# Kernel tuning notes

Hardware: AMD Instinct MI355X
Metric: run time of the kernel (lower is better)

Reference implementation:

```python
import jax, jax.numpy as jnp
import numpy as np

E = 768      # embedding_dim
H = 16       # max_heads
HD = E // H  # head_dim = 48


def setup_inputs() -> dict:
    key0 = jax.random.key(0)
    ks = jax.random.split(key0, 16)
    B, Lq, Lk = 4, 1024, 2048
    s = 0.02
    return {
        "query": jax.random.normal(ks[0], (B, Lq, E), jnp.float32),
        "key": jax.random.normal(ks[1], (B, Lk, E), jnp.float32),
        "value": jax.random.normal(ks[2], (B, Lk, E), jnp.float32),
        "key_padding_mask": jnp.zeros((B, Lk), jnp.bool_),
        # param_predictor: Linear(2E->E), Linear(E->E//2), Linear(E//2->3)
        "Wp1": jax.random.normal(ks[3], (E, 2 * E), jnp.float32) * s,
        "bp1": jnp.zeros((E,), jnp.float32),
        "Wp2": jax.random.normal(ks[4], (E // 2, E), jnp.float32) * s,
        "bp2": jnp.zeros((E // 2,), jnp.float32),
        "Wp3": jax.random.normal(ks[5], (3, E // 2), jnp.float32) * s,
        "bp3": jnp.zeros((3,), jnp.float32),
        # MultiheadAttention packed in-projection + out-projection
        "in_proj_w": jax.random.normal(ks[6], (3 * E, E), jnp.float32) * s,
        "in_proj_b": jnp.zeros((3 * E,), jnp.float32),
        "out_w": jax.random.normal(ks[7], (E, E), jnp.float32) * s,
        "out_b": jnp.zeros((E,), jnp.float32),
        # LayerNorm
        "ln_g": jnp.ones((E,), jnp.float32),
        "ln_b": jnp.zeros((E,), jnp.float32),
    }


def _layer_norm(x, g, b, eps=1e-5):
    mu = x.mean(-1, keepdims=True)
    var = ((x - mu) ** 2).mean(-1, keepdims=True)
    return (x - mu) * jax.lax.rsqrt(var + eps) * g + b


def reference(query, key, value, key_padding_mask,
              Wp1, bp1, Wp2, bp2, Wp3, bp3,
              in_proj_w, in_proj_b, out_w, out_b, ln_g, ln_b):
    B, Lq, _ = query.shape
    Lk = key.shape[1]

    # ---- dynamic parameter prediction MLP ----
    pin = jnp.concatenate([query.mean(1), key.mean(1)], axis=-1)  # [B, 2E]
    h = jax.nn.relu(pin @ Wp1.T + bp1)
    h = jax.nn.relu(h @ Wp2.T + bp2)
    pred = h @ Wp3.T + bp3                                        # [B, 3]
    num_heads = jnp.round(jax.nn.sigmoid(pred[:, 0]) * (H - 1) + 1).astype(jnp.int32)
    scale_factor = jax.nn.sigmoid(pred[:, 1]) * 0.5 + 0.5         # [B]
    gate_value = jax.nn.sigmoid(pred[:, 2])                       # [B]

    # ---- multihead cross-attention (non-flash: weights are materialized) ----
    q = query @ in_proj_w[:E].T + in_proj_b[:E]
    k = key @ in_proj_w[E:2 * E].T + in_proj_b[E:2 * E]
    v = value @ in_proj_w[2 * E:].T + in_proj_b[2 * E:]
    q = q.reshape(B, Lq, H, HD)
    k = k.reshape(B, Lk, H, HD)
    v = v.reshape(B, Lk, H, HD)
    scores = jnp.einsum('bqhd,bkhd->bhqk', q, k) / np.sqrt(HD)    # [B,H,Lq,Lk]
    scores = jnp.where(key_padding_mask[:, None, None, :], -1e30, scores)
    attn = jax.nn.softmax(scores, axis=-1)
    ctx = jnp.einsum('bhqk,bkhd->bqhd', attn, v).reshape(B, Lq, E)
    attn_output = ctx @ out_w.T + out_b
    attn_weights = attn.mean(1)                                   # avg over heads, [B,Lq,Lk]

    # ---- gated scale + residual + LayerNorm epilogue (dropout = eval/identity) ----
    sf = scale_factor[:, None, None]
    gv = gate_value[:, None, None]
    gated = query * (1.0 - gv) + (attn_output * sf) * gv
    output = _layer_norm(query + gated, ln_g, ln_b)
    return output, attn_weights, (num_heads, scale_factor, gate_value)
```

## Files before the change

kernel.cpp:

```cpp
#include <hip/hip_runtime.h>

#define B_ 4
#define LQ 1024
#define LK 2048
#define E_ 768
#define H_ 16
#define HD_ 48
#define HDP 64

#define OUT0_SIZE (B_*LQ*E_)
#define AW_OFF    (OUT0_SIZE)
#define AW_SIZE   (B_*LQ*LK)
#define NH_OFF    (AW_OFF + AW_SIZE)
#define SF_OFF    (NH_OFF + 4)
#define GV_OFF    (NH_OFF + 8)

#define WOFF_PIN    0
#define WOFF_QFRAG  49152
#define WOFF_KFRAG  (WOFF_QFRAG + (size_t)B_*H_*LQ*HDP*2)
#define WOFF_VFRAG  (WOFF_KFRAG + (size_t)B_*H_*LK*HDP*2)
#define WOFF_CTX    (WOFF_VFRAG + (size_t)B_*H_*HD_*LK*2)
#define WOFF_DINV   (WOFF_CTX + (size_t)B_*LQ*E_*2)
#define WOFF_H1     (WOFF_DINV + (size_t)B_*H_*LQ*4)
#define WOFF_H2     (WOFF_H1 + B_*E_*4)
#define WOFF_WBF    (WOFF_H2 + B_*(E_/2)*4)
#define WOFF_OWBF   (WOFF_WBF + (size_t)2304*768*2)
#define WOFF_AO     (WOFF_OWBF + (size_t)768*768*2)
#define WOFF_VBF    WOFF_AO
#define WS_SMALL    (WOFF_AO + (size_t)B_*LQ*E_*4)
#define WOFF_QBF    WS_SMALL
#define WOFF_KBF    (WOFF_QBF + (size_t)B_*LQ*E_*2)
#define WS_FULL     (WOFF_KBF + (size_t)B_*LK*E_*2)
#define WS_ZERO_BYTES WOFF_VFRAG

typedef unsigned short u16;
typedef __attribute__((ext_vector_type(8))) short short8;
typedef __attribute__((ext_vector_type(4))) short short4v;
typedef __attribute__((ext_vector_type(4))) float floatx4;

#define SC2 0.20823506544914194f
#define MFMA16(a,b,c) __builtin_amdgcn_mfma_f32_16x16x32_bf16(a,b,c,0,0,0)

__device__ __forceinline__ u16 f2bf(float x) {
  union { float f; unsigned u; } v; v.f = x;
  unsigned r = v.u + 0x7fffu + ((v.u >> 16) & 1u);
  return (u16)(r >> 16);
}
__device__ __forceinline__ unsigned cvt_pk_bf16(float a, float b) {
  unsigned r;
  asm("v_cvt_pk_bf16_f32 %0, %1, %2" : "=v"(r) : "v"(a), "v"(b));
  return r;
}
__device__ __forceinline__ short8 ldfrag_f32(const float* p) {
  const float4* q4 = (const float4*)p;
  float4 a = q4[0], b = q4[1];
  short8 r;
  r[0]=(short)f2bf(a.x); r[1]=(short)f2bf(a.y); r[2]=(short)f2bf(a.z); r[3]=(short)f2bf(a.w);
  r[4]=(short)f2bf(b.x); r[5]=(short)f2bf(b.y); r[6]=(short)f2bf(b.z); r[7]=(short)f2bf(b.w);
  return r;
}
__device__ __forceinline__ short8 ldfrag_bf16(const u16* p) { return *(const short8*)p; }

__device__ __forceinline__ size_t qkfrag_idx(int bh, int ltiles, int tile,
                                             int half, int slot, int e) {
  return ((((size_t)bh*ltiles + tile)*2 + half)*64 + slot)*8 + e;
}

__global__ __launch_bounds__(256) void conv_frag_k(const float* __restrict__ src,
                                                   u16* __restrict__ dst) {
  __shared__ u16 ls[16][776];
  int tid = threadIdx.x;
  size_t base = (size_t)blockIdx.x * 16 * 768;
  #pragma unroll
  for (int j=0;j<12;j++) {
    int i4 = tid + j*256;
    int r = i4 / 192, c4 = i4 - r*192;
    float4 v = *(const float4*)(src + base + (size_t)r*768 + c4*4);
    ushort4 o;
    o.x = f2bf(v.x); o.y = f2bf(v.y); o.z = f2bf(v.z); o.w = f2bf(v.w);
    *(ushort4*)&ls[r][c4*4] = o;
  }
  __syncthreads();
  u16* db = dst + (size_t)blockIdx.x * 24 * 512;
  #pragma unroll
  for (int j=0;j<6;j++) {
    int cid = tid + j*256;
    int kt = cid >> 6, slot = cid & 63;
    int rr = slot & 15, qq = slot >> 4;
    *(short8*)(db + (size_t)(kt*64 + slot)*8) = *(const short8*)&ls[rr][kt*32 + qq*8];
  }
}

__global__ __launch_bounds__(256) void maskpad_k(const unsigned char* __restrict__ mask,
    u16* __restrict__ qfrag, u16* __restrict__ kfrag) {
  int tid = blockIdx.x*256 + threadIdx.x;
  if (tid < B_*H_*LQ) {
    int bh = tid >> 10, row = tid & (LQ-1);
    qfrag[qkfrag_idx(bh, LQ/16, row>>4, 1, 32 + (row&15), 0)] = 0x3F80;
  }
  int bh = tid >> 11, row = tid & (LK-1);
  if (mask[(size_t)(bh>>4)*LK + row])
    kfrag[qkfrag_idx(bh, LK/16, row>>4, 1, 32 + (row&15), 0)] = f2bf(-1e30f);
}

__global__ __launch_bounds__(256) void pool_k(const float* __restrict__ query,
                                              const float* __restrict__ key,
                                              float* __restrict__ pin) {
  int bid = blockIdx.x;
  const float* src; int Lrows, fofs, b, fc, lch;
  if (bid < 96) { b = bid/24; int r = bid%24; fc = r/8;  lch = r%8;  src=query; Lrows=LQ; fofs=0; }
  else { int id = bid-96; b = id/48; int r = id%48; fc = r/16; lch = r%16; src=key; Lrows=LK; fofs=E_; }
  int f = fc*256 + threadIdx.x;
  const float* p = src + ((size_t)b*Lrows + lch*128)*E_ + f;
  float s = 0.f;
  #pragma unroll 4
  for (int i=0;i<128;i++) s += p[(size_t)i*E_];
  atomicAdd(&pin[b*2*E_ + fofs + f], s);
}

__global__ __launch_bounds__(256) void mlp1_k(const float* __restrict__ pin,
    const float* __restrict__ Wp1, const float* __restrict__ bp1,
    float* __restrict__ h1) {
  __shared__ float sp[B_][2*E_];
  int tid = threadIdx.x;
  for (int j = tid; j < B_*2*E_; j += 256) {
    int b = j / (2*E_), c = j % (2*E_);
    sp[b][c] = pin[b*2*E_ + c] * (c < E_ ? (1.f/LQ) : (1.f/LK));
  }
  __syncthreads();
  int wv = tid >> 6, lane = tid & 63;
  int rbase = (blockIdx.x*4 + wv) * 4;
  for (int rr = 0; rr < 4; rr++) {
    int r = rbase + rr;
    const float* w = Wp1 + (size_t)r*(2*E_);
    float a0=0.f,a1=0.f,a2=0.f,a3=0.f;
    for (int i = lane; i < 2*E_; i += 64) {
      float wj = w[i];
      a0 += wj*sp[0][i]; a1 += wj*sp[1][i]; a2 += wj*sp[2][i]; a3 += wj*sp[3][i];
    }
    #pragma unroll
    for (int m=1;m<64;m<<=1){
      a0+=__shfl_xor(a0,m,64); a1+=__shfl_xor(a1,m,64);
      a2+=__shfl_xor(a2,m,64); a3+=__shfl_xor(a3,m,64);
    }
    if (lane == 0) {
      float bb = bp1[r];
      h1[0*E_+r]=fmaxf(a0+bb,0.f); h1[1*E_+r]=fmaxf(a1+bb,0.f);
      h1[2*E_+r]=fmaxf(a2+bb,0.f); h1[3*E_+r]=fmaxf(a3+bb,0.f);
    }
  }
}

__global__ __launch_bounds__(256) void mlp2_k(const float* __restrict__ h1,
    const float* __restrict__ Wp2, const float* __restrict__ bp2,
    float* __restrict__ h2) {
  __shared__ float sh[B_][E_];
  int tid = threadIdx.x;
  for (int j = tid; j < B_*E_; j += 256) sh[j/E_][j%E_] = h1[j];
  __syncthreads();
  int wv = tid >> 6, lane = tid & 63;
  int rbase = (blockIdx.x*4 + wv) * 4;
  for (int rr = 0; rr < 4; rr++) {
    int r = rbase + rr;
    const float* w = Wp2 + (size_t)r*E_;
    float a0=0.f,a1=0.f,a2=0.f,a3=0.f;
    for (int i = lane; i < E_; i += 64) {
      float wj = w[i];
      a0 += wj*sh[0][i]; a1 += wj*sh[1][i]; a2 += wj*sh[2][i]; a3 += wj*sh[3][i];
    }
    #pragma unroll
    for (int m=1;m<64;m<<=1){
      a0+=__shfl_xor(a0,m,64); a1+=__shfl_xor(a1,m,64);
      a2+=__shfl_xor(a2,m,64); a3+=__shfl_xor(a3,m,64);
    }
    if (lane == 0) {
      float bb = bp2[r];
      h2[0*(E_/2)+r]=fmaxf(a0+bb,0.f); h2[1*(E_/2)+r]=fmaxf(a1+bb,0.f);
      h2[2*(E_/2)+r]=fmaxf(a2+bb,0.f); h2[3*(E_/2)+r]=fmaxf(a3+bb,0.f);
    }
  }
}

__global__ __launch_bounds__(256) void mlp3_k(const float* __restrict__ h2,
    const float* __restrict__ Wp3, const float* __restrict__ bp3,
    float* __restrict__ out) {
  int tid = threadIdx.x, wv = tid >> 6, lane = tid & 63;
  float a0=0.f,a1=0.f,a2=0.f;
  for (int i = lane; i < E_/2; i += 64) {
    float x = h2[wv*(E_/2)+i];
    a0 += x*Wp3[i]; a1 += x*Wp3[(E_/2)+i]; a2 += x*Wp3[2*(E_/2)+i];
  }
  #pragma unroll
  for (int m=1;m<64;m<<=1){
    a0+=__shfl_xor(a0,m,64); a1+=__shfl_xor(a1,m,64); a2+=__shfl_xor(a2,m,64);
  }
  if (lane == 0) {
    float p0 = a0 + bp3[0], p1 = a1 + bp3[1], p2 = a2 + bp3[2];
    float s0 = 1.f/(1.f+expf(-p0));
    float s1 = 1.f/(1.f+expf(-p1));
    float s2 = 1.f/(1.f+expf(-p2));
    out[NH_OFF + wv] = rintf(s0*(H_-1) + 1.f);
    out[SF_OFF + wv] = s1*0.5f + 0.5f;
    out[GV_OFF + wv] = s2;
  }
}

template<int MODE, bool ABF, int TSH>
__global__ __launch_bounds__(256) void gemm_fm(const void* __restrict__ Ap,
    const u16* __restrict__ Bf, const float* __restrict__ bias,
    void* __restrict__ Cp, float cscale) {
  int lane = threadIdx.x & 63, wv = threadIdx.x >> 6;
  int lc = lane & 15, quad = lane >> 4;
  int lid = blockIdx.y * gridDim.x + blockIdx.x;
  int xcd = lid & 7, rr = lid >> 3;
  int C = gridDim.y >> 3;
  int lx = rr % gridDim.x, ly = xcd*C + rr / gridDim.x;
  int wm = ly*128 + (wv & 1)*64;
  int wn = lx*64  + (wv >> 1)*32;
  int mt0 = wm >> 4, nt0 = wn >> 4;
  const float* Af = (const float*)Ap;
  const u16*  Abf = (const u16*)Ap;
  floatx4 acc[4][2];
  #pragma unroll
  for (int s=0;s<4;s++)
    #pragma unroll
    for (int t=0;t<2;t++) acc[s][t] = (floatx4){0.f,0.f,0.f,0.f};
  #pragma unroll 2
  for (int kt=0; kt<24; kt++) {
    short8 af[4], bf2[2];
    #pragma unroll
    for (int s=0;s<4;s++)
      af[s] = ABF ? ldfrag_bf16(Abf + ((size_t)(mt0+s)*24 + kt)*512 + lane*8)
                  : ldfrag_f32(Af + (size_t)(wm + s*16 + lc)*E_ + kt*32 + quad*8);
    #pragma unroll
    for (int t=0;t<2;t++)
      bf2[t] = ldfrag_bf16(Bf + ((size_t)(nt0+t)*24 + kt)*512 + lane*8);
    #pragma unroll
    for (int s=0;s<4;s++)
      #pragma unroll
      for (int t=0;t<2;t++)
        acc[s][t] = MFMA16(af[s], bf2[t], acc[s][t]);
  }
  #pragma unroll
  for (int s=0;s<4;s++)
    #pragma unroll
    for (int t=0;t<2;t++)
      #pragma unroll
      for (int r=0;r<4;r++) {
        int m = wm + s*16 + quad*4 + r;
        int n = wn + t*16 + lc;
        float v = (acc[s][t][r] + bias[n]) * cscale;
        if (MODE == 0) {
          ((float*)Cp)[(size_t)m*E_ + n] = v;
        } else if (MODE == 1) {
          int bi = m >> TSH, l = m & ((1<<TSH)-1);
          int hh = n / HD_, d = n - hh*HD_;
          int half = d >> 5, q2 = (d >> 3) & 3, e = d & 7;
          ((u16*)Cp)[qkfrag_idx(bi*H_+hh, (1<<TSH)>>4, l>>4, half, q2*16 + (l&15), e)]
            = f2bf(v);
        } else {
          int bi = m >> 11, kc = m & 2047;
          int hh = n / HD_, d = n - hh*HD_;
          int dt = d >> 4, nn = d & 15;
          int kt2 = kc >> 6, c0 = (kc >> 5) & 1, q2 = (kc >> 3) & 3, e = kc & 7;
          size_t idx = ((((size_t)(bi*H_+hh)*(LK/64) + kt2)*3 + dt)*2 + c0)*512
                       + (q2*16+nn)*8 + e;
          ((u16*)Cp)[idx] = f2bf(v);
        }
      }
}

__global__ __launch_bounds__(512) void attn_fused_k(const u16* __restrict__ qfrag,
    const u16* __restrict__ kfrag, const u16* __restrict__ vfrag,
    float* __restrict__ dinv, u16* __restrict__ ctxb) {
  __shared__ __align__(16) u16 lp[8][16][72];
  __shared__ float cacc[4][64][33];
  int lane = threadIdx.x & 63, wv = threadIdx.x >> 6;
  int wq = wv & 3, kw = wv >> 2;
  int lc = lane & 15, quad = lane >> 4;
  int b = blockIdx.z, h = blockIdx.y, bh = b*H_ + h;
  int qw0 = blockIdx.x*128 + wq*32;
  const u16* qb = qfrag + (size_t)bh*(LQ/16)*1024;
  const u16* kb = kfrag + (size_t)bh*(LK/16)*1024;
  const u16* vb = vfrag + (size_t)bh*(LK/64)*3072;
  short8 qf[2][2];
  #pragma unroll
  for (int qt=0;qt<2;qt++)
    #pragma unroll
    for (int hf=0;hf<2;hf++)
      qf[qt][hf] = ldfrag_bf16(qb + (((qw0>>4)+qt)*2 + hf)*512 + lane*8);
  floatx4 lv[2];
  lv[0] = (floatx4){0.f,0.f,0.f,0.f}; lv[1] = lv[0];
  floatx4 acc[2][3];
  #pragma unroll
  for (int qt=0;qt<2;qt++)
    #pragma unroll
    for (int dt=0;dt<3;dt++) acc[qt][dt] = (floatx4){0.f,0.f,0.f,0.f};

  int kend = (kw + 1) << 10;
  for (int k0 = kw << 10; k0 < kend; k0 += 64) {
    short8 kf[4][2];
    #pragma unroll
    for (int t=0;t<4;t++)
      #pragma unroll
      for (int hf=0;hf<2;hf++)
        kf[t][hf] = ldfrag_bf16(kb + (((k0>>4)+t)*2 + hf)*512 + lane*8);
    short8 vf[2][3];
    #pragma unroll
    for (int c0=0;c0<2;c0++)
      #pragma unroll
      for (int dt=0;dt<3;dt++)
        vf[c0][dt] = ldfrag_bf16(vb + (((k0>>6)*3 + dt)*2 + c0)*512 + lane*8);

    #pragma unroll
    for (int qt=0;qt<2;qt++) {
      #pragma unroll
      for (int t=0;t<4;t++) {
        floatx4 z = {0.f,0.f,0.f,0.f};
        floatx4 st = MFMA16(kf[t][0], qf[qt][0], MFMA16(kf[t][1], qf[qt][1], z));
        floatx4 p;
        #pragma unroll
        for (int r=0;r<4;r++) p[r] = __builtin_amdgcn_exp2f(st[r]);
        lv[qt] += p;
        uint2 pk2;
        pk2.x = cvt_pk_bf16(p[0], p[1]);
        pk2.y = cvt_pk_bf16(p[2], p[3]);
        *(uint2*)&lp[wv][lc][t*16 + quad*4] = pk2;
      }
      short8 pa0 = *(const short8*)&lp[wv][lc][quad*8];
      short8 pa1 = *(const short8*)&lp[wv][lc][32 + quad*8];
      #pragma unroll
      for (int dt=0;dt<3;dt++)
        acc[qt][dt] = MFMA16(pa1, vf[1][dt], MFMA16(pa0, vf[0][dt], acc[qt][dt]));
    }
  }
  float l0 = lv[0][0]+lv[0][1]+lv[0][2]+lv[0][3];
  float l1 = lv[1][0]+lv[1][1]+lv[1][2]+lv[1][3];
  if (kw) {
    float* cb = &cacc[wq][lane][0];
    #pragma unroll
    for (int qt=0;qt<2;qt++)
      #pragma unroll
      for (int dt=0;dt<3;dt++)
        #pragma unroll
        for (int r=0;r<4;r++) cb[(qt*3+dt)*4 + r] = acc[qt][dt][r];
    cb[24] = l0; cb[25] = l1;
  }
  __syncthreads();
  if (kw) return;
  {
    const float* cb = &cacc[wq][lane][0];
    #pragma unroll
    for (int qt=0;qt<2;qt++)
      #pragma unroll
      for (int dt=0;dt<3;dt++)
        #pragma unroll
        for (int r=0;r<4;r++) acc[qt][dt][r] += cb[(qt*3+dt)*4 + r];
    l0 += cb[24]; l1 += cb[25];
  }
  float lq[2] = {l0, l1};
  #pragma unroll
  for (int qt=0;qt<2;qt++) {
    float s = lq[qt];
    s += __shfl_xor(s, 16, 64);
    s += __shfl_xor(s, 32, 64);
    float linv = 1.f/s;
    if (lane < 16) dinv[(size_t)bh*LQ + qw0 + qt*16 + lane] = linv;
    float li[4];
    #pragma unroll
    for (int r=0;r<4;r++) li[r] = __shfl(linv, quad*4 + r, 64);
    #pragma unroll
    for (int dt=0;dt<3;dt++)
      #pragma unroll
      for (int r=0;r<4;r++) {
        int mg = b*LQ + qw0 + qt*16 + quad*4 + r;
        int k  = h*HD_ + dt*16 + lc;
        size_t idx = (((size_t)(mg>>4)*(E_/32) + (k>>5))*64 + ((k>>3)&3)*16 + (mg&15))*8 + (k&7);
        ctxb[idx] = f2bf(acc[qt][dt][r]*li[r]);
      }
  }
}

__global__ __launch_bounds__(256) void attn_weights_k(const u16* __restrict__ qfrag,
    const u16* __restrict__ kfrag, const float* __restrict__ dinv,
    float* __restrict__ aw) {
  int lane = threadIdx.x & 63, wv = threadIdx.x >> 6;
  int lc = lane & 15, quad = lane >> 4;
  int b = blockIdx.z;
  int qw0 = blockIdx.y*64 + (wv & 1)*32;
  int k0  = blockIdx.x*64 + (wv >> 1)*32;
  floatx4 acc[2][2];
  #pragma unroll
  for (int qt=0;qt<2;qt++)
    #pragma unroll
    for (int t=0;t<2;t++) acc[qt][t] = (floatx4){0.f,0.f,0.f,0.f};
  for (int h=0;h<H_;h++) {
    int bh = b*H_ + h;
    const u16* qb = qfrag + (size_t)bh*(LQ/16)*1024;
    const u16* kb = kfrag + (size_t)bh*(LK/16)*1024;
    short8 qf[2][2];
    float di[2];
    #pragma unroll
    for (int qt=0;qt<2;qt++) {
      #pragma unroll
      for (int hf=0;hf<2;hf++)
        qf[qt][hf] = ldfrag_bf16(qb + (((qw0>>4)+qt)*2 + hf)*512 + lane*8);
      di[qt] = dinv[(size_t)bh*LQ + qw0 + qt*16 + lc];
    }
    short8 kf[2][2];
    #pragma unroll
    for (int t=0;t<2;t++)
      #pragma unroll
      for (int hf=0;hf<2;hf++)
        kf[t][hf] = ldfrag_bf16(kb + (((k0>>4)+t)*2 + hf)*512 + lane*8);
    #pragma unroll
    for (int qt=0;qt<2;qt++)
      #pragma unroll
      for (int t=0;t<2;t++) {
        floatx4 z = {0.f,0.f,0.f,0.f};
        floatx4 st = MFMA16(kf[t][0], qf[qt][0], MFMA16(kf[t][1], qf[qt][1], z));
        #pragma unroll
        for (int r=0;r<4;r++)
          acc[qt][t][r] += __builtin_amdgcn_exp2f(st[r]) * di[qt];
      }
  }
  const float inv16 = 1.f/16.f;
  #pragma unroll
  for (int qt=0;qt<2;qt++)
    #pragma unroll
    for (int t=0;t<2;t++) {
      floatx4 v = acc[qt][t];
      v[0]*=inv16; v[1]*=inv16; v[2]*=inv16; v[3]*=inv16;
      *(floatx4*)&aw[((size_t)b*LQ + qw0 + qt*16 + lc)*LK + k0 + t*16 + quad*4] = v;
    }
}

__global__ __launch_bounds__(256) void final_ln_k(const float* __restrict__ query,
    const float* __restrict__ ao, const float* __restrict__ lng,
    const float* __restrict__ lnb, float* __restrict__ out) {
  int row = blockIdx.x, b = row >> 10, tid = threadIdx.x;
  float sf = out[SF_OFF + b];
  float gv = out[GV_OFF + b];
  float c1 = 2.f - gv, c2 = sf*gv;
  const float* q = query + (size_t)row*E_;
  const float* a = ao + (size_t)row*E_;
  float x[3], s1 = 0.f, s2 = 0.f;
  #pragma unroll
  for (int i=0;i<3;i++){ int j = tid + i*256; float v = q[j]*c1 + a[j]*c2; x[i]=v; s1+=v; s2+=v*v; }
  #pragma unroll
  for (int m=1;m<64;m<<=1){ s1 += __shfl_xor(s1,m,64); s2 += __shfl_xor(s2,m,64); }
  __shared__ float r1[4], r2[4];
  int wv = tid >> 6;
  if ((tid & 63) == 0){ r1[wv]=s1; r2[wv]=s2; }
  __syncthreads();
  s1 = r1[0]+r1[1]+r1[2]+r1[3];
  s2 = r2[0]+r2[1]+r2[2]+r2[3];
  float mu = s1*(1.f/E_);
  float var = s2*(1.f/E_) - mu*mu;
  float rs = rsqrtf(var + 1e-5f);
  #pragma unroll
  for (int i=0;i<3;i++){ int j = tid + i*256; out[(size_t)row*E_ + j] = (x[i]-mu)*rs*lng[j] + lnb[j]; }
}

extern "C" void kernel_launch(void* const* d_in, const int* in_sizes, int n_in,
                              void* d_out, int out_size, void* d_ws, size_t ws_size,
                              hipStream_t stream) {
  const float* query = (const float*)d_in[0];
  const float* key   = (const float*)d_in[1];
  const float* value = (const float*)d_in[2];
  const unsigned char* mask = (const unsigned char*)d_in[3];
  const float* Wp1 = (const float*)d_in[4];
  const float* bp1 = (const float*)d_in[5];
  const float* Wp2 = (const float*)d_in[6];
  const float* bp2 = (const float*)d_in[7];
  const float* Wp3 = (const float*)d_in[8];
  const float* bp3 = (const float*)d_in[9];
  const float* ipw = (const float*)d_in[10];
  const float* ipb = (const float*)d_in[11];
  const float* outw = (const float*)d_in[12];
  const float* outb = (const float*)d_in[13];
  const float* lng = (const float*)d_in[14];
  const float* lnb = (const float*)d_in[15];
  float* out = (float*)d_out;
  char* ws = (char*)d_ws;
  if (ws_size < WS_SMALL) return;
  bool full = (ws_size >= WS_FULL);
  float* pin  = (float*)(ws + WOFF_PIN);
  u16* qfrag  = (u16*)(ws + WOFF_QFRAG);
  u16* kfrag  = (u16*)(ws + WOFF_KFRAG);
  u16* vfrag  = (u16*)(ws + WOFF_VFRAG);
  u16* ctxb   = (u16*)(ws + WOFF_CTX);
  float* dinv = (float*)(ws + WOFF_DINV);
  float* h1   = (float*)(ws + WOFF_H1);
  float* h2   = (float*)(ws + WOFF_H2);
  u16* wbf    = (u16*)(ws + WOFF_WBF);
  u16* owbf   = (u16*)(ws + WOFF_OWBF);
  float* ao   = (float*)(ws + WOFF_AO);
  u16* vbf    = (u16*)(ws + WOFF_VBF);
  u16* qbf    = (u16*)(ws + WOFF_QBF);
  u16* kbf    = (u16*)(ws + WOFF_KBF);

  hipMemsetAsync(ws, 0, WS_ZERO_BYTES, stream);
  maskpad_k<<<512, 256, 0, stream>>>(mask, qfrag, kfrag);
  pool_k<<<288, 256, 0, stream>>>(query, key, pin);
  mlp1_k<<<48, 256, 0, stream>>>(pin, Wp1, bp1, h1);
  mlp2_k<<<24, 256, 0, stream>>>(h1, Wp2, bp2, h2);
  mlp3_k<<<1, 256, 0, stream>>>(h2, Wp3, bp3, out);

  conv_frag_k<<<144, 256, 0, stream>>>(ipw, wbf);
  conv_frag_k<<<48, 256, 0, stream>>>(outw, owbf);
  const u16* wq = wbf;
  const u16* wk = wbf + (size_t)48*24*512;
  const u16* wvv = wbf + (size_t)96*24*512;
  if (full) {
    conv_frag_k<<<256, 256, 0, stream>>>(query, qbf);
    conv_frag_k<<<512, 256, 0, stream>>>(key, kbf);
    conv_frag_k<<<512, 256, 0, stream>>>(value, vbf);
    gemm_fm<1,true,10><<<dim3(12,32), 256, 0, stream>>>((const void*)qbf, wq, ipb, (void*)qfrag, SC2);
    gemm_fm<1,true,11><<<dim3(12,64), 256, 0, stream>>>((const void*)kbf, wk, ipb + E_, (void*)kfrag, 1.f);
    gemm_fm<2,true,11><<<dim3(12,64), 256, 0, stream>>>((const void*)vbf, wvv, ipb + 2*E_, (void*)vfrag, 1.f);
  } else {
    gemm_fm<1,false,10><<<dim3(12,32), 256, 0, stream>>>((const void*)query, wq, ipb, (void*)qfrag, SC2);
    gemm_fm<1,false,11><<<dim3(12,64), 256, 0, stream>>>((const void*)key, wk, ipb + E_, (void*)kfrag, 1.f);
    gemm_fm<2,false,11><<<dim3(12,64), 256, 0, stream>>>((const void*)value, wvv, ipb + 2*E_, (void*)vfrag, 1.f);
  }
  attn_fused_k<<<dim3(8,16,4), 512, 0, stream>>>(qfrag, kfrag, vfrag, dinv, ctxb);
  attn_weights_k<<<dim3(32,16,4), 256, 0, stream>>>(qfrag, kfrag, dinv, out + AW_OFF);
  gemm_fm<0,true,10><<<dim3(12,32), 256, 0, stream>>>((const void*)ctxb, owbf, outb, (void*)ao, 1.f);
  final_ln_k<<<4096, 256, 0, stream>>>(query, ao, lng, lnb, out);
}
```

Baseline: 421.9 us.

## Stage Q/K fragments in double-buffered LDS with larger tiles in attn_weights

Rewrites the attention-weights kernel to use 512-thread blocks covering 128x128 (q,k) tiles. Each head's Q and K fragments are cooperatively loaded into double-buffered shared memory, with the next head's loads issued into registers before the current head's compute. Per-wave work grows to 4 q-tiles by 2 k-tiles, and the launch becomes a 1D grid whose block index is decoded so that neighbouring blocks map across XCDs. The aim is more fragment reuse and less redundant global/L2 traffic, paid for with two barriers per head, more LDS and more registers.

```diff
diff --git a/kernel.cpp b/kernel.cpp
--- a/kernel.cpp
+++ b/kernel.cpp
@@ -381,52 +381,94 @@
   }
 }
 
-__global__ __launch_bounds__(256) void attn_weights_k(const u16* __restrict__ qfrag,
+#define AW_QSTR ((LQ/16)*1024)
+#define AW_KSTR ((LK/16)*1024)
+
+__global__ __launch_bounds__(512) void attn_weights_k(const u16* __restrict__ qfrag,
     const u16* __restrict__ kfrag, const float* __restrict__ dinv,
     float* __restrict__ aw) {
-  int lane = threadIdx.x & 63, wv = threadIdx.x >> 6;
+  __shared__ __align__(16) u16 sq[2][8192];
+  __shared__ __align__(16) u16 sk[2][8192];
+  int tid = threadIdx.x;
+  int lane = tid & 63, wv = tid >> 6;
   int lc = lane & 15, quad = lane >> 4;
-  int b = blockIdx.z;
-  int qw0 = blockIdx.y*64 + (wv & 1)*32;
-  int k0  = blockIdx.x*64 + (wv >> 1)*32;
-  floatx4 acc[2][2];
-  #pragma unroll
-  for (int qt=0;qt<2;qt++)
+  int xcd = blockIdx.x & 7, rest = blockIdx.x >> 3;
+  int kx = rest & 15, g3 = rest >> 4;
+  int y = xcd, b = g3;
+  int qblk = y*128, kblk = kx*128;
+  int wq = wv & 1, wk = wv >> 1;
+  int qw0 = qblk + wq*64;
+  int k0  = kblk + wk*32;
+  const u16* qb0 = qfrag + (size_t)(b*H_)*AW_QSTR + (qblk>>4)*1024;
+  const u16* kb0 = kfrag + (size_t)(b*H_)*AW_KSTR + (kblk>>4)*1024;
+  const float* dv0 = dinv + (size_t)(b*H_)*LQ + qw0;
+  floatx4 acc[4][2];
+  #pragma unroll
+  for (int qt=0;qt<4;qt++)
     #pragma unroll
     for (int t=0;t<2;t++) acc[qt][t] = (floatx4){0.f,0.f,0.f,0.f};
-  for (int h=0;h<H_;h++) {
-    int bh = b*H_ + h;
-    const u16* qb = qfrag + (size_t)bh*(LQ/16)*1024;
-    const u16* kb = kfrag + (size_t)bh*(LK/16)*1024;
-    short8 qf[2][2];
-    float di[2];
-    #pragma unroll
-    for (int qt=0;qt<2;qt++) {
+
+  short8 gq[2], gk[2];
+  #pragma unroll
+  for (int i=0;i<2;i++) {
+    gq[i] = *(const short8*)(qb0 + (size_t)(tid + i*512)*8);
+    gk[i] = *(const short8*)(kb0 + (size_t)(tid + i*512)*8);
+  }
+  #pragma unroll
+  for (int i=0;i<2;i++) {
+    *(short8*)&sq[0][(tid + i*512)*8] = gq[i];
+    *(short8*)&sk[0][(tid + i*512)*8] = gk[i];
+  }
+  __syncthreads();
+
+  for (int h=0; h<H_; h++) {
+    int cur = h & 1;
+    if (h+1 < H_) {
+      const u16* qbn = qb0 + (size_t)(h+1)*AW_QSTR;
+      const u16* kbn = kb0 + (size_t)(h+1)*AW_KSTR;
+      #pragma unroll
+      for (int i=0;i<2;i++) {
+        gq[i] = *(const short8*)(qbn + (size_t)(tid + i*512)*8);
+        gk[i] = *(const short8*)(kbn + (size_t)(tid + i*512)*8);
+      }
+    }
+    float di[4];
+    const float* dvh = dv0 + (size_t)h*LQ;
+    #pragma unroll
+    for (int qt=0;qt<4;qt++) di[qt] = dvh[qt*16 + lc];
+    short8 kf[2][2];
+    #pragma unroll
+    for (int t=0;t<2;t++)
       #pragma unroll
       for (int hf=0;hf<2;hf++)
-        qf[qt][hf] = ldfrag_bf16(qb + (((qw0>>4)+qt)*2 + hf)*512 + lane*8);
-      di[qt] = dinv[(size_t)bh*LQ + qw0 + qt*16 + lc];
-    }
-    short8 kf[2][2];
-    #pragma unroll
-    for (int t=0;t<2;t++)
-      #pragma unroll
-      for (int hf=0;hf<2;hf++)
-        kf[t][hf] = ldfrag_bf16(kb + (((k0>>4)+t)*2 + hf)*512 + lane*8);
-    #pragma unroll
-    for (int qt=0;qt<2;qt++)
+        kf[t][hf] = *(const short8*)&sk[cur][(((wk*2+t)*2+hf)*64 + lane)*8];
+    #pragma unroll
+    for (int qt=0;qt<4;qt++) {
+      short8 qf0 = *(const short8*)&sq[cur][(((wq*4+qt)*2+0)*64 + lane)*8];
+      short8 qf1 = *(const short8*)&sq[cur][(((wq*4+qt)*2+1)*64 + lane)*8];
       #pragma unroll
       for (int t=0;t<2;t++) {
         floatx4 z = {0.f,0.f,0.f,0.f};
-        floatx4 st = MFMA16(kf[t][0], qf[qt][0], MFMA16(kf[t][1], qf[qt][1], z));
+        floatx4 st = MFMA16(kf[t][0], qf0, MFMA16(kf[t][1], qf1, z));
         #pragma unroll
         for (int r=0;r<4;r++)
           acc[qt][t][r] += __builtin_amdgcn_exp2f(st[r]) * di[qt];
       }
+    }
+    __syncthreads();
+    if (h+1 < H_) {
+      int nxt = cur ^ 1;
+      #pragma unroll
+      for (int i=0;i<2;i++) {
+        *(short8*)&sq[nxt][(tid + i*512)*8] = gq[i];
+        *(short8*)&sk[nxt][(tid + i*512)*8] = gk[i];
+      }
+    }
+    __syncthreads();
   }
   const float inv16 = 1.f/16.f;
   #pragma unroll
-  for (int qt=0;qt<2;qt++)
+  for (int qt=0;qt<4;qt++)
     #pragma unroll
     for (int t=0;t<2;t++) {
       floatx4 v = acc[qt][t];
@@ -525,7 +567,7 @@
     gemm_fm<2,false,11><<<dim3(12,64), 256, 0, stream>>>((const void*)value, wvv, ipb + 2*E_, (void*)vfrag, 1.f);
   }
   attn_fused_k<<<dim3(8,16,4), 512, 0, stream>>>(qfrag, kfrag, vfrag, dinv, ctxb);
-  attn_weights_k<<<dim3(32,16,4), 256, 0, stream>>>(qfrag, kfrag, dinv, out + AW_OFF);
+  attn_weights_k<<<512, 512, 0, stream>>>(qfrag, kfrag, dinv, out + AW_OFF);
   gemm_fm<0,true,10><<<dim3(12,32), 256, 0, stream>>>((const void*)ctxb, owbf, outb, (void*)ao, 1.f);
   final_ln_k<<<4096, 256, 0, stream>>>(query, ao, lng, lnb, out);
 }
```

After: 406.9 us. -3.6%, faster.
